# Kernel optimization log

Measured on AMD Instinct MI355X. Metric: run time of the kernel, lower is better.

Reference implementation:

```python
import jax, jax.numpy as jnp
import numpy as np
import math

C, F, NH, W = 8, 256, 8, 1024  # channels, features (h), num_heads, frames (w)


def conv3x3(x, w):
    # x: [b,c,h,w], w: [out_c,in_c,3,3], padding=1, stride=1, no bias
    return jax.lax.conv_general_dilated(
        x, w, window_strides=(1, 1), padding=((1, 1), (1, 1)),
        dimension_numbers=("NCHW", "OIHW", "NCHW"))


def mc_linear_pw(x, w_pw):
    # per-channel linear over the feature (h) axis
    # x: [b,c,h,w], w_pw: [c, h_out, h_in] -> [b,c,h_out,w]
    return jnp.einsum("bchw,cgh->bcgw", x, w_pw)


def setup_inputs() -> dict:
    key = jax.random.key(0)
    ks = jax.random.split(key, 11)
    conv_s = 1.0 / math.sqrt(C * 9)
    pw_s = 1.0 / math.sqrt(F)
    dw_s = 1.0 / math.sqrt(C)
    return {
        "x": jax.random.normal(ks[0], (1, C, F, W), jnp.float32),
        "prev_qk": jax.random.normal(ks[1], (1, C, NH, W, W), jnp.float32),
        "wq_conv": jax.random.normal(ks[2], (C, C, 3, 3), jnp.float32) * conv_s,
        "wk_conv": jax.random.normal(ks[3], (C, C, 3, 3), jnp.float32) * conv_s,
        "wv_conv": jax.random.normal(ks[4], (C, C, 3, 3), jnp.float32) * conv_s,
        "wq_pw": jax.random.normal(ks[5], (C, F, F), jnp.float32) * pw_s,
        "wk_pw": jax.random.normal(ks[6], (C, F, F), jnp.float32) * pw_s,
        "wv_pw": jax.random.normal(ks[7], (C, F, F), jnp.float32) * pw_s,
        "wo_dw": jax.random.normal(ks[8], (C, C), jnp.float32) * dw_s,
        "wo_pw": jax.random.normal(ks[9], (C, F, F), jnp.float32) * pw_s,
    }


def reference(x, prev_qk, wq_conv, wk_conv, wv_conv, wq_pw, wk_pw, wv_pw, wo_dw, wo_pw):
    b, c, h, w = x.shape
    dh = h // NH

    def proj_heads(inp, w_conv, w_pw):
        p = mc_linear_pw(conv3x3(inp, w_conv), w_pw)          # [b,c,h,w]
        p = jnp.transpose(p, (0, 1, 3, 2))                     # [b,c,w,h]
        p = p.reshape(b, c, w, NH, dh)                         # [b,c,w,nh,dh]
        return jnp.transpose(p, (0, 1, 3, 2, 4))               # [b,c,nh,w,dh]

    q = proj_heads(x, wq_conv, wq_pw)
    k = proj_heads(x, wk_conv, wk_pw)
    v = proj_heads(x, wv_conv, wv_pw)

    # attention in fp32 over the frame (w) axis, scaled by sqrt(h) (features)
    qk = jnp.einsum("bcnqd,bcnkd->bcnqk", q.astype(jnp.float32), k.astype(jnp.float32)) / math.sqrt(h)
    qk = qk + prev_qk
    a = jnp.einsum("bcnqk,bcnkd->bcnqd", jax.nn.softmax(qk, axis=-1), v.astype(jnp.float32))
    a = jnp.transpose(a, (0, 1, 3, 2, 4)).reshape(b, c, w, h)  # [b,c,w,h]
    a = jnp.transpose(a, (0, 1, 3, 2))                          # [b,c,h,w]

    # o_proj: depthwise channel mix then per-channel positionwise linear
    o = jnp.einsum("bchw,dc->bdhw", a, wo_dw)
    out = mc_linear_pw(o, wo_pw)
    return (out, qk)
```

## Files before the change

kernel.cpp:

```cpp
#include <hip/hip_runtime.h>
#include <hip/hip_bf16.h>


typedef float f32x4 __attribute__((ext_vector_type(4)));
typedef short s16x8 __attribute__((ext_vector_type(8)));

static __device__ __forceinline__ unsigned short f2bf(float f) {
  unsigned int u = __builtin_bit_cast(unsigned int, f);
  u += 0x7fff + ((u >> 16) & 1);
  return (unsigned short)(u >> 16);
}

__global__ __launch_bounds__(256) void cvt_weights(
    const float* __restrict__ wq, const float* __restrict__ wk,
    const float* __restrict__ wv, const float* __restrict__ wo,
    unsigned short* __restrict__ dst) {
  int gid = blockIdx.x * 256 + threadIdx.x;
  int e = gid * 4;
  int arr = e >> 19;
  int off = e & 524287;
  const float* src = arr == 0 ? wq : arr == 1 ? wk : arr == 2 ? wv : wo;
  float4 v = *(const float4*)(src + off);
  ushort4 o;
  o.x = f2bf(v.x); o.y = f2bf(v.y); o.z = f2bf(v.z); o.w = f2bf(v.w);
  *(ushort4*)(dst + (size_t)arr * 524288 + off) = o;
}

__global__ __launch_bounds__(256) void conv3x3_k(
    const float* __restrict__ x,
    const float* __restrict__ wq, const float* __restrict__ wk,
    const float* __restrict__ wv,
    unsigned short* __restrict__ convT) {
  __shared__ float xt[8][34][36];
  int t = blockIdx.z;
  const float* wc = (t == 0) ? wq : (t == 1) ? wk : wv;
  int wtile = blockIdx.x * 32, htile = blockIdx.y * 32;
  int tid = threadIdx.x;
  for (int i = tid; i < 8 * 34 * 34; i += 256) {
    int cp = i / 1156;
    int rem = i - cp * 1156;
    int hh = rem / 34, ww = rem - hh * 34;
    int gh = htile + hh - 1, gw = wtile + ww - 1;
    float v = 0.f;
    if ((unsigned)gh < 256u && (unsigned)gw < 1024u)
      v = x[((size_t)cp * 256 + gh) * 1024 + gw];
    xt[cp][hh][ww] = v;
  }
  __syncthreads();
  int tx = tid & 31, strip = tid >> 5;
  int h0 = strip * 4;
  float acc[8][4];
#pragma unroll
  for (int co = 0; co < 8; ++co)
#pragma unroll
    for (int p = 0; p < 4; ++p) acc[co][p] = 0.f;
#pragma unroll 1
  for (int cp = 0; cp < 8; ++cp) {
    float xv[6][3];
#pragma unroll
    for (int rr = 0; rr < 6; ++rr)
#pragma unroll
      for (int cc = 0; cc < 3; ++cc)
        xv[rr][cc] = xt[cp][h0 + rr][tx + cc];
#pragma unroll
    for (int i = 0; i < 3; ++i)
#pragma unroll
      for (int j = 0; j < 3; ++j) {
#pragma unroll
        for (int co = 0; co < 8; ++co) {
          float wgt = wc[((co * 8 + cp) * 3 + i) * 3 + j];
#pragma unroll
          for (int p = 0; p < 4; ++p)
            acc[co][p] += wgt * xv[p + i][j];
        }
      }
  }
  int w = wtile + tx;
#pragma unroll
  for (int co = 0; co < 8; ++co) {
    ushort4 o;
    o.x = f2bf(acc[co][0]); o.y = f2bf(acc[co][1]);
    o.z = f2bf(acc[co][2]); o.w = f2bf(acc[co][3]);
    *(ushort4*)(convT + ((size_t)(t * 8 + co) * 1024 + w) * 256 + htile + h0) = o;
  }
}

__global__ __launch_bounds__(256) void gemm_pw(
    const unsigned short* __restrict__ A0,
    const unsigned short* __restrict__ B0,
    unsigned short* __restrict__ qkh,
    unsigned short* __restrict__ vstd,
    float* __restrict__ outp,
    int mode) {
  int b = blockIdx.z;
  const unsigned short* A = A0 + (size_t)b * 65536;
  const unsigned short* B = B0 + (size_t)b * 262144;
  int lane = threadIdx.x & 63, wvid = threadIdx.x >> 6;
  int wm = wvid & 1, wn = wvid >> 1;
  int mBase = blockIdx.y * 128 + wm * 64;
  int nBase = blockIdx.x * 128 + wn * 64;
  int c15 = lane & 15, klo = (lane >> 4) * 8;
  f32x4 acc[4][4];
#pragma unroll
  for (int mi = 0; mi < 4; ++mi)
#pragma unroll
    for (int ni = 0; ni < 4; ++ni) acc[mi][ni] = (f32x4){0.f, 0.f, 0.f, 0.f};
#pragma unroll 2
  for (int kk = 0; kk < 256; kk += 32) {
    s16x8 af[4], bf[4];
#pragma unroll
    for (int mi = 0; mi < 4; ++mi)
      af[mi] = *(const s16x8*)(A + (size_t)(mBase + mi * 16 + c15) * 256 + kk + klo);
#pragma unroll
    for (int ni = 0; ni < 4; ++ni)
      bf[ni] = *(const s16x8*)(B + (size_t)(nBase + ni * 16 + c15) * 256 + kk + klo);
#pragma unroll
    for (int mi = 0; mi < 4; ++mi)
#pragma unroll
      for (int ni = 0; ni < 4; ++ni)
        acc[mi][ni] = __builtin_amdgcn_mfma_f32_16x16x32_bf16(
            af[mi], bf[ni], acc[mi][ni], 0, 0, 0);
  }
  int r0 = (lane >> 4) * 4;
  if (mode == 0) {
    int t = b >> 3, c = b & 7;
    if (t < 2) {
      unsigned short* dst = qkh + (size_t)t * 2097152 + (size_t)c * 262144;
#pragma unroll
      for (int mi = 0; mi < 4; ++mi)
#pragma unroll
        for (int ni = 0; ni < 4; ++ni) {
          int g = mBase + mi * 16 + r0;
          int w = nBase + ni * 16 + c15;
          int n = g >> 5, d = g & 31;
          ushort4 o;
          o.x = f2bf(acc[mi][ni][0]); o.y = f2bf(acc[mi][ni][1]);
          o.z = f2bf(acc[mi][ni][2]); o.w = f2bf(acc[mi][ni][3]);
          *(ushort4*)(dst + ((size_t)n * 1024 + w) * 32 + d) = o;
        }
    } else {
      unsigned short* dst = vstd + (size_t)c * 262144;
#pragma unroll
      for (int mi = 0; mi < 4; ++mi)
#pragma unroll
        for (int ni = 0; ni < 4; ++ni) {
          int w = nBase + ni * 16 + c15;
#pragma unroll
          for (int r = 0; r < 4; ++r)
            dst[(size_t)(mBase + mi * 16 + r0 + r) * 1024 + w] = f2bf(acc[mi][ni][r]);
        }
    }
  } else {
    float* dst = outp + (size_t)b * 262144;
#pragma unroll
    for (int mi = 0; mi < 4; ++mi)
#pragma unroll
      for (int ni = 0; ni < 4; ++ni) {
        int w = nBase + ni * 16 + c15;
#pragma unroll
        for (int r = 0; r < 4; ++r)
          dst[(size_t)(mBase + mi * 16 + r0 + r) * 1024 + w] = acc[mi][ni][r];
      }
  }
}

__global__ __launch_bounds__(256, 2) void attn_k(
    const unsigned short* __restrict__ Qh,
    const unsigned short* __restrict__ Kh,
    const unsigned short* __restrict__ Vstd,
    const float* __restrict__ prev,
    float* __restrict__ qkOut,
    float* __restrict__ aOut) {
  __shared__ char ldsRaw[4][16384];
  int lane = threadIdx.x & 63, wvid = threadIdx.x >> 6;
  int cn = blockIdx.y;
  int c = cn >> 3, n = cn & 7;
  int qBase = blockIdx.x * 64 + wvid * 16;
  int c15 = lane & 15, quad = lane >> 4, klo = quad * 8;
  const unsigned short* Q = Qh + (size_t)cn * 32768;
  const unsigned short* K = Kh + (size_t)cn * 32768;
  const unsigned short* V = Vstd + (size_t)c * 262144 + (size_t)n * 32768;
  char* base = ldsRaw[wvid];
  const float* prevB = prev + (size_t)cn * 1048576;
  float* qkB = qkOut + (size_t)cn * 1048576;
  s16x8 qf = *(const s16x8*)(Q + (size_t)(qBase + c15) * 32 + klo);
  f32x4 o0 = {0.f, 0.f, 0.f, 0.f}, o1 = {0.f, 0.f, 0.f, 0.f};
  float lsum[16];
#pragma unroll
  for (int r = 0; r < 16; ++r) lsum[r] = 0.f;

#pragma unroll 1
  for (int kb = 0; kb < 1024; kb += 256) {
#pragma unroll
    for (int kt = 0; kt < 16; ++kt) {
      s16x8 kf = *(const s16x8*)(K + (size_t)(kb + kt * 16 + c15) * 32 + klo);
      f32x4 z = {0.f, 0.f, 0.f, 0.f};
      f32x4 s2 = __builtin_amdgcn_mfma_f32_16x16x32_bf16(kf, qf, z, 0, 0, 0);
      *(f32x4*)(base + c15 * 1024 + (((kt * 4 + quad) ^ (c15 & 7)) << 4)) = s2;
    }
#pragma unroll
    for (int r = 0; r < 16; ++r) {
      f32x4 sv = *(const f32x4*)(base + r * 1024 + ((lane ^ (r & 7)) << 4));
      f32x4 pv = *(const f32x4*)(prevB + (size_t)(qBase + r) * 1024 + kb + lane * 4);
      f32x4 val = sv * 0.0625f + pv;
      __builtin_nontemporal_store(val,
          (f32x4*)(qkB + (size_t)(qBase + r) * 1024 + kb + lane * 4));
      float p0 = __expf(val[0]), p1 = __expf(val[1]),
            p2 = __expf(val[2]), p3 = __expf(val[3]);
      lsum[r] += (p0 + p1) + (p2 + p3);
      ushort4 pk;
      pk.x = f2bf(p0); pk.y = f2bf(p1); pk.z = f2bf(p2); pk.w = f2bf(p3);
      *(ushort4*)(base + r * 1024 + 512 +
                  ((((lane >> 1) ^ (r & 7)) << 4) | ((lane & 1) << 3))) = pk;
    }
#pragma unroll
    for (int kk2 = 0; kk2 < 8; ++kk2) {
      s16x8 pf = *(const s16x8*)(base + c15 * 1024 + 512 +
                                 ((((kk2 * 4 + quad) ^ (c15 & 7)) << 4)));
      s16x8 v0 = *(const s16x8*)(V + (size_t)c15 * 1024 + kb + kk2 * 32 + klo);
      s16x8 v1 = *(const s16x8*)(V + (size_t)(16 + c15) * 1024 + kb + kk2 * 32 + klo);
      o0 = __builtin_amdgcn_mfma_f32_16x16x32_bf16(pf, v0, o0, 0, 0, 0);
      o1 = __builtin_amdgcn_mfma_f32_16x16x32_bf16(pf, v1, o1, 0, 0, 0);
    }
  }
  float* swf = (float*)base;
#pragma unroll
  for (int r = 0; r < 16; ++r) {
    float t = lsum[r];
    t += __shfl_xor(t, 1);  t += __shfl_xor(t, 2);
    t += __shfl_xor(t, 4);  t += __shfl_xor(t, 8);
    t += __shfl_xor(t, 16); t += __shfl_xor(t, 32);
    if (lane == 0) swf[r] = t;
  }
#pragma unroll
  for (int rr = 0; rr < 4; ++rr) {
    float inv = 1.0f / swf[quad * 4 + rr];
    int q = qBase + quad * 4 + rr;
    aOut[((size_t)c * 256 + n * 32 + c15) * 1024 + q] = o0[rr] * inv;
    aOut[((size_t)c * 256 + n * 32 + 16 + c15) * 1024 + q] = o1[rr] * inv;
  }
}

__global__ __launch_bounds__(256) void mix_t(
    const float* __restrict__ a, const float* __restrict__ dw,
    unsigned short* __restrict__ ot) {
  int tx = threadIdx.x & 31, strip = threadIdx.x >> 5;
  int wtile = blockIdx.x * 32, htile = blockIdx.y * 32;
  int w = wtile + tx, h0 = htile + strip * 4;
  float acc[8][4];
#pragma unroll
  for (int co = 0; co < 8; ++co)
#pragma unroll
    for (int p = 0; p < 4; ++p) acc[co][p] = 0.f;
#pragma unroll 1
  for (int cp = 0; cp < 8; ++cp) {
    float av[4];
#pragma unroll
    for (int p = 0; p < 4; ++p)
      av[p] = a[((size_t)cp * 256 + h0 + p) * 1024 + w];
#pragma unroll
    for (int co = 0; co < 8; ++co) {
      float wgt = dw[co * 8 + cp];
#pragma unroll
      for (int p = 0; p < 4; ++p) acc[co][p] += wgt * av[p];
    }
  }
#pragma unroll
  for (int co = 0; co < 8; ++co) {
    ushort4 o;
    o.x = f2bf(acc[co][0]); o.y = f2bf(acc[co][1]);
    o.z = f2bf(acc[co][2]); o.w = f2bf(acc[co][3]);
    *(ushort4*)(ot + ((size_t)co * 1024 + w) * 256 + h0) = o;
  }
}

extern "C" void kernel_launch(void* const* d_in, const int* in_sizes, int n_in,
                              void* d_out, int out_size, void* d_ws, size_t ws_size,
                              hipStream_t stream) {
  (void)in_sizes; (void)n_in; (void)out_size; (void)ws_size;
  const float* x       = (const float*)d_in[0];
  const float* prev    = (const float*)d_in[1];
  const float* wq_conv = (const float*)d_in[2];
  const float* wk_conv = (const float*)d_in[3];
  const float* wv_conv = (const float*)d_in[4];
  const float* wq_pw   = (const float*)d_in[5];
  const float* wk_pw   = (const float*)d_in[6];
  const float* wv_pw   = (const float*)d_in[7];
  const float* wo_dw   = (const float*)d_in[8];
  const float* wo_pw   = (const float*)d_in[9];

  float* outp  = (float*)d_out;
  float* qkOut = outp + 2097152;

  char* ws = (char*)d_ws;
  unsigned short* pwB   = (unsigned short*)ws;
  unsigned short* convT = (unsigned short*)(ws + (4  << 20));
  unsigned short* qkh   = (unsigned short*)(ws + (16 << 20));
  unsigned short* vstd  = (unsigned short*)(ws + (24 << 20));
  float*          aBuf  = (float*)         (ws + (28 << 20));
  unsigned short* otB   = (unsigned short*)(ws + (36 << 20));

  cvt_weights<<<2048, 256, 0, stream>>>(wq_pw, wk_pw, wv_pw, wo_pw, pwB);
  conv3x3_k<<<dim3(32, 8, 3), 256, 0, stream>>>(x, wq_conv, wk_conv, wv_conv, convT);
  gemm_pw<<<dim3(8, 2, 24), 256, 0, stream>>>(pwB, convT, qkh, vstd, nullptr, 0);
  attn_k<<<dim3(16, 64), 256, 0, stream>>>(qkh, qkh + 2097152, vstd, prev, qkOut, aBuf);
  mix_t<<<dim3(32, 8), 256, 0, stream>>>(aBuf, wo_dw, otB);
  gemm_pw<<<dim3(8, 2, 8), 256, 0, stream>>>(pwB + 3 * 524288, otB, nullptr, nullptr, outp, 1);
}
```

Before: 646.3 us.

## Split attention key axis across waves with cross-wave reduction per 16-query block

Each block now handles 16 queries instead of 64, and its four waves split the 1024-key axis, each covering 256 keys. Waves write partial PV outputs and row sums to shared memory, which are then reduced across waves. The grid grows fourfold, and prev_qk loads are prefetched one row ahead. The qk store becomes a regular store instead of a nontemporal one. This adds block barriers and 64KB of LDS per block, which may limit occupancy, and K/V tiles are now read by four times as many blocks.

```diff
diff --git a/kernel.cpp b/kernel.cpp
--- a/kernel.cpp
+++ b/kernel.cpp
@@ -171,74 +171,102 @@
     const float* __restrict__ prev,
     float* __restrict__ qkOut,
     float* __restrict__ aOut) {
-  __shared__ char ldsRaw[4][16384];
-  int lane = threadIdx.x & 63, wvid = threadIdx.x >> 6;
+  __shared__ __align__(16) float sT[16384];
+  int lane = threadIdx.x & 63, w = threadIdx.x >> 6;
   int cn = blockIdx.y;
   int c = cn >> 3, n = cn & 7;
-  int qBase = blockIdx.x * 64 + wvid * 16;
+  int qBase = blockIdx.x * 16;
   int c15 = lane & 15, quad = lane >> 4, klo = quad * 8;
   const unsigned short* Q = Qh + (size_t)cn * 32768;
   const unsigned short* K = Kh + (size_t)cn * 32768;
   const unsigned short* V = Vstd + (size_t)c * 262144 + (size_t)n * 32768;
-  char* base = ldsRaw[wvid];
-  const float* prevB = prev + (size_t)cn * 1048576;
-  float* qkB = qkOut + (size_t)cn * 1048576;
+  const float* prevB = prev + (size_t)cn * 1048576 + (size_t)qBase * 1024;
+  float* qkB = qkOut + (size_t)cn * 1048576 + (size_t)qBase * 1024;
+
   s16x8 qf = *(const s16x8*)(Q + (size_t)(qBase + c15) * 32 + klo);
+
+#pragma unroll
+  for (int kt = 0; kt < 16; ++kt) {
+    s16x8 kf = *(const s16x8*)(K + (size_t)(w * 256 + kt * 16 + c15) * 32 + klo);
+    f32x4 z = {0.f, 0.f, 0.f, 0.f};
+    f32x4 s2 = __builtin_amdgcn_mfma_f32_16x16x32_bf16(kf, qf, z, 0, 0, 0);
+    *(f32x4*)(sT + c15 * 1024 + (((w * 64 + kt * 4 + quad) ^ (c15 & 7)) << 2)) = s2;
+  }
+  __syncthreads();
+
+  float lsums[4] = {0.f, 0.f, 0.f, 0.f};
+  {
+    int q0 = 4 * w;
+    f32x4 pv[4], pvN[4];
+#pragma unroll
+    for (int p = 0; p < 4; ++p)
+      pv[p] = *(const f32x4*)(prevB + (size_t)q0 * 1024 + p * 256 + lane * 4);
+#pragma unroll
+    for (int jr = 0; jr < 4; ++jr) {
+      int q = q0 + jr;
+      if (jr < 3) {
+#pragma unroll
+        for (int p = 0; p < 4; ++p)
+          pvN[p] = *(const f32x4*)(prevB + (size_t)(q + 1) * 1024 + p * 256 + lane * 4);
+      }
+#pragma unroll
+      for (int p = 0; p < 4; ++p) {
+        f32x4 sv = *(const f32x4*)(sT + q * 1024 + (((p * 64 + lane) ^ (q & 7)) << 2));
+        f32x4 val = sv * 0.0625f + pv[p];
+        *(f32x4*)(qkB + (size_t)q * 1024 + p * 256 + lane * 4) = val;
+        float e0 = __expf(val[0]), e1 = __expf(val[1]),
+              e2 = __expf(val[2]), e3 = __expf(val[3]);
+        lsums[jr] += (e0 + e1) + (e2 + e3);
+        ushort4 pk;
+        pk.x = f2bf(e0); pk.y = f2bf(e1); pk.z = f2bf(e2); pk.w = f2bf(e3);
+        *(ushort4*)((char*)sT + q * 4096 +
+                    (((p * 32 + (lane >> 1)) ^ (q & 7)) << 4) + ((lane & 1) << 3)) = pk;
+      }
+#pragma unroll
+      for (int p = 0; p < 4; ++p) pv[p] = pvN[p];
+    }
+  }
+  __syncthreads();
+
   f32x4 o0 = {0.f, 0.f, 0.f, 0.f}, o1 = {0.f, 0.f, 0.f, 0.f};
-  float lsum[16];
-#pragma unroll
-  for (int r = 0; r < 16; ++r) lsum[r] = 0.f;
-
-#pragma unroll 1
-  for (int kb = 0; kb < 1024; kb += 256) {
-#pragma unroll
-    for (int kt = 0; kt < 16; ++kt) {
-      s16x8 kf = *(const s16x8*)(K + (size_t)(kb + kt * 16 + c15) * 32 + klo);
-      f32x4 z = {0.f, 0.f, 0.f, 0.f};
-      f32x4 s2 = __builtin_amdgcn_mfma_f32_16x16x32_bf16(kf, qf, z, 0, 0, 0);
-      *(f32x4*)(base + c15 * 1024 + (((kt * 4 + quad) ^ (c15 & 7)) << 4)) = s2;
-    }
-#pragma unroll
-    for (int r = 0; r < 16; ++r) {
-      f32x4 sv = *(const f32x4*)(base + r * 1024 + ((lane ^ (r & 7)) << 4));
-      f32x4 pv = *(const f32x4*)(prevB + (size_t)(qBase + r) * 1024 + kb + lane * 4);
-      f32x4 val = sv * 0.0625f + pv;
-      __builtin_nontemporal_store(val,
-          (f32x4*)(qkB + (size_t)(qBase + r) * 1024 + kb + lane * 4));
-      float p0 = __expf(val[0]), p1 = __expf(val[1]),
-            p2 = __expf(val[2]), p3 = __expf(val[3]);
-      lsum[r] += (p0 + p1) + (p2 + p3);
-      ushort4 pk;
-      pk.x = f2bf(p0); pk.y = f2bf(p1); pk.z = f2bf(p2); pk.w = f2bf(p3);
-      *(ushort4*)(base + r * 1024 + 512 +
-                  ((((lane >> 1) ^ (r & 7)) << 4) | ((lane & 1) << 3))) = pk;
-    }
-#pragma unroll
-    for (int kk2 = 0; kk2 < 8; ++kk2) {
-      s16x8 pf = *(const s16x8*)(base + c15 * 1024 + 512 +
-                                 ((((kk2 * 4 + quad) ^ (c15 & 7)) << 4)));
-      s16x8 v0 = *(const s16x8*)(V + (size_t)c15 * 1024 + kb + kk2 * 32 + klo);
-      s16x8 v1 = *(const s16x8*)(V + (size_t)(16 + c15) * 1024 + kb + kk2 * 32 + klo);
-      o0 = __builtin_amdgcn_mfma_f32_16x16x32_bf16(pf, v0, o0, 0, 0, 0);
-      o1 = __builtin_amdgcn_mfma_f32_16x16x32_bf16(pf, v1, o1, 0, 0, 0);
-    }
-  }
-  float* swf = (float*)base;
-#pragma unroll
-  for (int r = 0; r < 16; ++r) {
-    float t = lsum[r];
+#pragma unroll
+  for (int j = 0; j < 8; ++j) {
+    s16x8 pf = *(const s16x8*)((char*)sT + c15 * 4096 +
+                               (((w * 32 + j * 4 + quad) ^ (c15 & 7)) << 4));
+    s16x8 v0 = *(const s16x8*)(V + (size_t)c15 * 1024 + w * 256 + j * 32 + klo);
+    s16x8 v1 = *(const s16x8*)(V + (size_t)(16 + c15) * 1024 + w * 256 + j * 32 + klo);
+    o0 = __builtin_amdgcn_mfma_f32_16x16x32_bf16(pf, v0, o0, 0, 0, 0);
+    o1 = __builtin_amdgcn_mfma_f32_16x16x32_bf16(pf, v1, o1, 0, 0, 0);
+  }
+#pragma unroll
+  for (int jr = 0; jr < 4; ++jr) {
+    float t = lsums[jr];
     t += __shfl_xor(t, 1);  t += __shfl_xor(t, 2);
     t += __shfl_xor(t, 4);  t += __shfl_xor(t, 8);
     t += __shfl_xor(t, 16); t += __shfl_xor(t, 32);
-    if (lane == 0) swf[r] = t;
-  }
-#pragma unroll
-  for (int rr = 0; rr < 4; ++rr) {
-    float inv = 1.0f / swf[quad * 4 + rr];
-    int q = qBase + quad * 4 + rr;
-    aOut[((size_t)c * 256 + n * 32 + c15) * 1024 + q] = o0[rr] * inv;
-    aOut[((size_t)c * 256 + n * 32 + 16 + c15) * 1024 + q] = o1[rr] * inv;
-  }
+    lsums[jr] = t;
+  }
+  __syncthreads();
+  float* opart = sT;
+  float* lsumArr = sT + 2048;
+  *(f32x4*)(opart + w * 512 + c15 * 16 + quad * 4) = o0;
+  *(f32x4*)(opart + w * 512 + (16 + c15) * 16 + quad * 4) = o1;
+  if (lane == 0) {
+    lsumArr[4 * w + 0] = lsums[0];
+    lsumArr[4 * w + 1] = lsums[1];
+    lsumArr[4 * w + 2] = lsums[2];
+    lsumArr[4 * w + 3] = lsums[3];
+  }
+  __syncthreads();
+  int q = threadIdx.x & 15, d = threadIdx.x >> 4;
+  float inv = 1.0f / lsumArr[q];
+  float s0 = opart[d * 16 + q] + opart[512 + d * 16 + q] +
+             opart[1024 + d * 16 + q] + opart[1536 + d * 16 + q];
+  int d1 = d + 16;
+  float s1 = opart[d1 * 16 + q] + opart[512 + d1 * 16 + q] +
+             opart[1024 + d1 * 16 + q] + opart[1536 + d1 * 16 + q];
+  aOut[((size_t)(c * 256 + n * 32 + d)) * 1024 + qBase + q] = s0 * inv;
+  aOut[((size_t)(c * 256 + n * 32 + d1)) * 1024 + qBase + q] = s1 * inv;
 }
 
 __global__ __launch_bounds__(256) void mix_t(
@@ -303,7 +331,7 @@
   cvt_weights<<<2048, 256, 0, stream>>>(wq_pw, wk_pw, wv_pw, wo_pw, pwB);
   conv3x3_k<<<dim3(32, 8, 3), 256, 0, stream>>>(x, wq_conv, wk_conv, wv_conv, convT);
   gemm_pw<<<dim3(8, 2, 24), 256, 0, stream>>>(pwB, convT, qkh, vstd, nullptr, 0);
-  attn_k<<<dim3(16, 64), 256, 0, stream>>>(qkh, qkh + 2097152, vstd, prev, qkOut, aBuf);
+  attn_k<<<dim3(64, 64), 256, 0, stream>>>(qkh, qkh + 2097152, vstd, prev, qkOut, aBuf);
   mix_t<<<dim3(32, 8), 256, 0, stream>>>(aBuf, wo_dw, otB);
   gemm_pw<<<dim3(8, 2, 8), 256, 0, stream>>>(pwB + 3 * 524288, otB, nullptr, nullptr, outp, 1);
 }
```

Result: faster. 539.7 us (-16.5%).
